# Optimization experiments

Measured on AMD Instinct MI355X. Metric: run time of the kernel, lower is better.

Reference implementation:

```python
import jax, jax.numpy as jnp
import numpy as np

N_INIT = jnp.array([17.047, 14.099, 3.625], dtype=jnp.float32)
CA_INIT = jnp.array([16.967, 12.784, 4.338], dtype=jnp.float32)
C_INIT = jnp.array([15.685, 12.755, 5.133], dtype=jnp.float32)


def _unit(x):
    return x / (jnp.linalg.norm(x, axis=-1, keepdims=True) + 1e-8)


def _place_dihedral(a, b, c, bond_angle, bond_length, torsion):
    # a,b,c: [B,3]; bond_angle/bond_length/torsion: [B]
    ab = b - a
    bc = _unit(c - b)
    cr = jnp.cross(ab, bc)
    crn = jnp.linalg.norm(cr, axis=-1, keepdims=True)
    n_main = _unit(cr)
    # collinear fallback (per-element; almost never triggers for real angles)
    perp = jnp.zeros_like(bc).at[..., 0].set(1.0)
    ct = jnp.cross(bc, perp)
    ctn = jnp.linalg.norm(ct, axis=-1, keepdims=True)
    perp2 = jnp.where(ctn < 1e-6, jnp.zeros_like(bc).at[..., 1].set(1.0), perp)
    n_fb = _unit(jnp.cross(bc, perp2))
    n = jnp.where(crn < 1e-6, n_fb, n_main)
    nbc = jnp.cross(n, bc)
    m = jnp.stack([bc, nbc, n], axis=-1)  # [B,3,3]
    d_local = jnp.stack([
        -bond_length * jnp.cos(bond_angle),
        bond_length * jnp.cos(torsion) * jnp.sin(bond_angle),
        bond_length * jnp.sin(torsion) * jnp.sin(bond_angle),
    ], axis=-1)  # [B,3]
    d = jnp.einsum('bij,bj->bi', m, d_local)
    return d + c


def _nerf_build(phi, psi, omega, bond_lengths, bond_angles):
    B, L = phi.shape
    init = jnp.broadcast_to(jnp.stack([N_INIT, CA_INIT, C_INIT]), (B, 3, 3))
    # per-step params, leading axis = residue index i in [0, L-2]
    xs = (
        psi[:, :L - 1].T,                 # psi_i
        omega[:, :L - 1].T,               # omega_i
        phi[:, 1:].T,                     # phi_{i+1}
        bond_lengths[:, :L - 1, 2].T,     # C-N length
        bond_lengths[:, :L - 1, 0].T,     # N-CA length
        bond_lengths[:, :L - 1, 1].T,     # CA-C length
        bond_angles[:, :L - 1, 1].T,      # CA-C-N angle
        bond_angles[:, :L - 1, 2].T,      # C-N-CA angle
        bond_angles[:, :L - 1, 0].T,      # N-CA-C angle
    )

    def step(prev, x):
        psi_i, omega_i, phi_i, len_cn, len_nca, len_cac, ang_cacn, ang_cnca, ang_ncac = x
        a, b, c = prev[:, 0], prev[:, 1], prev[:, 2]
        n = _place_dihedral(a, b, c, ang_cacn, len_cn, psi_i)
        ca = _place_dihedral(b, c, n, ang_cnca, len_nca, omega_i)
        cc = _place_dihedral(c, n, ca, ang_ncac, len_cac, phi_i)
        new = jnp.stack([n, ca, cc], axis=1)  # [B,3,3]
        return new, new

    _, outs = jax.lax.scan(step, init, xs)  # [L-1,B,3,3]
    rest = outs.transpose(1, 0, 2, 3).reshape(B, 3 * (L - 1), 3)
    return jnp.concatenate([init, rest], axis=1)  # [B, 3L, 3]


def setup_inputs() -> dict:
    key = jax.random.key(0)
    k0, k1, k2, k3, k4 = jax.random.split(key, 5)
    B, L = 4096, 512
    phi = jax.random.normal(k0, (B, L), dtype=jnp.float32)
    psi = jax.random.normal(k1, (B, L), dtype=jnp.float32)
    omega = jax.random.normal(k2, (B, L), dtype=jnp.float32)
    # realistic positive bond lengths (~1.0-1.5 A) and bond angles (~1.5-2.3 rad)
    bond_lengths = 1.0 + 0.5 * jax.random.uniform(k3, (B, L, 3), dtype=jnp.float32)
    bond_angles = 1.5 + 0.8 * jax.random.uniform(k4, (B, L, 3), dtype=jnp.float32)
    return {"phi": phi, "psi": psi, "omega": omega,
            "bond_lengths": bond_lengths, "bond_angles": bond_angles}


def reference(phi, psi, omega, bond_lengths, bond_angles):
    return _nerf_build(phi, psi, omega, bond_lengths, bond_angles)
```

## Files before the change

### kernel.cpp

```cpp
#include <hip/hip_runtime.h>
#include <math.h>


#define LCH 512

struct Xf { float r[9]; float t[3]; };

__device__ __forceinline__ Xf xf_compose(const Xf& A, const Xf& B) {
  Xf C;
#pragma unroll
  for (int i = 0; i < 3; ++i) {
    float a0 = A.r[3*i+0], a1 = A.r[3*i+1], a2 = A.r[3*i+2];
    C.r[3*i+0] = a0*B.r[0] + a1*B.r[3] + a2*B.r[6];
    C.r[3*i+1] = a0*B.r[1] + a1*B.r[4] + a2*B.r[7];
    C.r[3*i+2] = a0*B.r[2] + a1*B.r[5] + a2*B.r[8];
    C.t[i]     = a0*B.t[0] + a1*B.t[1] + a2*B.t[2] + A.t[i];
  }
  return C;
}

__device__ __forceinline__ void xf_step(Xf& P, float theta, float len, float tau) {
  float st, ct, sx, cx;
  __sincosf(theta, &st, &ct);
  __sincosf(tau, &sx, &cx);
  float ux = -ct, uy = cx*st, uz = sx*st;
  float v0 = -st, v1 = -ct*cx, v2 = -ct*sx;
  float c00 = P.r[0]*ux + P.r[1]*uy + P.r[2]*uz;
  float c10 = P.r[3]*ux + P.r[4]*uy + P.r[5]*uz;
  float c20 = P.r[6]*ux + P.r[7]*uy + P.r[8]*uz;
  float c01 = P.r[0]*v0 + P.r[1]*v1 + P.r[2]*v2;
  float c11 = P.r[3]*v0 + P.r[4]*v1 + P.r[5]*v2;
  float c21 = P.r[6]*v0 + P.r[7]*v1 + P.r[8]*v2;
  float c02 = P.r[2]*cx - P.r[1]*sx;
  float c12 = P.r[5]*cx - P.r[4]*sx;
  float c22 = P.r[8]*cx - P.r[7]*sx;
  P.t[0] += len*c00; P.t[1] += len*c10; P.t[2] += len*c20;
  P.r[0]=c00; P.r[1]=c01; P.r[2]=c02;
  P.r[3]=c10; P.r[4]=c11; P.r[5]=c12;
  P.r[6]=c20; P.r[7]=c21; P.r[8]=c22;
}

__device__ __forceinline__ void xf_set_delta(Xf& P, float theta, float len, float tau) {
  float st, ct, sx, cx;
  __sincosf(theta, &st, &ct);
  __sincosf(tau, &sx, &cx);
  float ux = -ct, uy = cx*st, uz = sx*st;
  P.r[0]=ux; P.r[1]=-st;    P.r[2]=0.f;
  P.r[3]=uy; P.r[4]=-ct*cx; P.r[5]=-sx;
  P.r[6]=uz; P.r[7]=-ct*sx; P.r[8]=cx;
  P.t[0]=len*ux; P.t[1]=len*uy; P.t[2]=len*uz;
}

__device__ __forceinline__ void xf_identity(Xf& A) {
  A.r[0]=1.f; A.r[1]=0.f; A.r[2]=0.f;
  A.r[3]=0.f; A.r[4]=1.f; A.r[5]=0.f;
  A.r[6]=0.f; A.r[7]=0.f; A.r[8]=1.f;
  A.t[0]=0.f; A.t[1]=0.f; A.t[2]=0.f;
}

__device__ __forceinline__ Xf xf_shfl_up(const Xf& P, int d) {
  Xf O;
#pragma unroll
  for (int i = 0; i < 9; ++i) O.r[i] = __shfl_up(P.r[i], d, 64);
#pragma unroll
  for (int i = 0; i < 3; ++i) O.t[i] = __shfl_up(P.t[i], d, 64);
  return O;
}

#define REP(f) (A.r[3*((f)%3)+0]*sx[(f)/3] + A.r[3*((f)%3)+1]*sy[(f)/3] \
              + A.r[3*((f)%3)+2]*sz[(f)/3] + A.t[(f)%3])

__global__ __launch_bounds__(128) void nerf_r14_kernel(
    const float* __restrict__ g_phi, const float* __restrict__ g_psi,
    const float* __restrict__ g_omg, const float* __restrict__ g_bl,
    const float* __restrict__ g_ba, float* __restrict__ g_out)
{
  __shared__ float s_tot[12];
  __shared__ float s_out[4608];

  const int t    = threadIdx.x;
  const int lane = t & 63;
  const int wave = t >> 6;
  const int chain = blockIdx.x;

  const float* phir = g_phi + (size_t)chain * LCH;
  const float* psir = g_psi + (size_t)chain * LCH;
  const float* omgr = g_omg + (size_t)chain * LCH;
  const float* blr  = g_bl  + (size_t)chain * (LCH*3);
  const float* bar  = g_ba  + (size_t)chain * (LCH*3);

  const int j4  = 4 * t;
  const int b12 = 12 * t;

  float4 vps = *(const float4*)(psir + j4);
  float4 vom = *(const float4*)(omgr + j4);
  float4 vph = *(const float4*)(phir + j4);
  float4 l0  = *(const float4*)(blr + b12);
  float4 l1  = *(const float4*)(blr + b12 + 4);
  float4 l2  = *(const float4*)(blr + b12 + 8);
  float4 a0  = *(const float4*)(bar + b12);
  float4 a1  = *(const float4*)(bar + b12 + 4);
  float4 a2  = *(const float4*)(bar + b12 + 8);

  float psN  = __shfl_up(vps.w, 1, 64);
  float omN  = __shfl_up(vom.w, 1, 64);
  float blN0 = __shfl_up(l2.y, 1, 64);
  float blN1 = __shfl_up(l2.z, 1, 64);
  float blN2 = __shfl_up(l2.w, 1, 64);
  float baN0 = __shfl_up(a2.y, 1, 64);
  float baN1 = __shfl_up(a2.z, 1, 64);
  float baN2 = __shfl_up(a2.w, 1, 64);
  if (lane == 0 && t != 0) {
    psN  = psir[j4 - 1];
    omN  = omgr[j4 - 1];
    blN0 = blr[b12 - 3]; blN1 = blr[b12 - 2]; blN2 = blr[b12 - 1];
    baN0 = bar[b12 - 3]; baN1 = bar[b12 - 2]; baN2 = bar[b12 - 1];
  }

  float PS[4] = { psN, vps.x, vps.y, vps.z };
  float OM[4] = { omN, vom.x, vom.y, vom.z };
  float PH[4] = { vph.x, vph.y, vph.z, vph.w };
  float BL[12] = { blN0, blN1, blN2, l0.x, l0.y, l0.z, l0.w,
                   l1.x, l1.y, l1.z, l1.w, l2.x };
  float BA[12] = { baN0, baN1, baN2, a0.x, a0.y, a0.z, a0.w,
                   a1.x, a1.y, a1.z, a1.w, a2.x };

  Xf P;
  float sx[12], sy[12], sz[12];
#pragma unroll
  for (int k = 0; k < 12; ++k) {
    const int m = k / 3, a = k - 3*m;
    float th, ln, ta;
    if (a == 0)      { th = BA[3*m+1]; ln = BL[3*m+2]; ta = PS[m]; }
    else if (a == 1) { th = BA[3*m+2]; ln = BL[3*m+0]; ta = OM[m]; }
    else             { th = BA[3*m+0]; ln = BL[3*m+1]; ta = PH[m]; }
    if (k == 0) xf_set_delta(P, th, ln, ta);
    else        xf_step(P, th, ln, ta);
    sx[k] = P.t[0]; sy[k] = P.t[1]; sz[k] = P.t[2];
    if (k == 2 && t == 0) xf_identity(P);
  }

#pragma unroll
  for (int d = 1; d < 64; d <<= 1) {
    Xf O = xf_shfl_up(P, d);
    if (lane >= d) P = xf_compose(O, P);
  }

  if (wave == 0 && lane == 63) {
#pragma unroll
    for (int i = 0; i < 9; ++i) s_tot[i] = P.r[i];
#pragma unroll
    for (int i = 0; i < 3; ++i) s_tot[9+i] = P.t[i];
  }
  Xf E = xf_shfl_up(P, 1);
  __syncthreads();

  Xf A;
  {
    const float ax=17.047f, ay=14.099f, az=3.625f;
    const float bx_=16.967f, by_=12.784f, bz_=4.338f;
    const float cx_=15.685f, cy_=12.755f, cz_=5.133f;
    float abx=bx_-ax, aby=by_-ay, abz=bz_-az;
    float vx=cx_-bx_, vy=cy_-by_, vz=cz_-bz_;
    float vn = sqrtf(vx*vx+vy*vy+vz*vz) + 1e-8f;
    vx/=vn; vy/=vn; vz/=vn;
    float crx = aby*vz - abz*vy;
    float cry = abz*vx - abx*vz;
    float crz = abx*vy - aby*vx;
    float cn = sqrtf(crx*crx+cry*cry+crz*crz) + 1e-8f;
    float nx=crx/cn, ny=cry/cn, nz=crz/cn;
    float mx = ny*vz - nz*vy;
    float my = nz*vx - nx*vz;
    float mz = nx*vy - ny*vx;
    A.r[0]=vx; A.r[1]=mx; A.r[2]=nx;
    A.r[3]=vy; A.r[4]=my; A.r[5]=ny;
    A.r[6]=vz; A.r[7]=mz; A.r[8]=nz;
    A.t[0]=cx_; A.t[1]=cy_; A.t[2]=cz_;
  }
  if (wave == 1) {
    Xf T;
#pragma unroll
    for (int i = 0; i < 9; ++i) T.r[i] = s_tot[i];
#pragma unroll
    for (int i = 0; i < 3; ++i) T.t[i] = s_tot[9+i];
    A = xf_compose(A, T);
  }
  if (lane > 0) A = xf_compose(A, E);

#pragma unroll
  for (int q = 0; q < 9; ++q) {
    float4 v;
    v.x = REP(4*q + 0);
    v.y = REP(4*q + 1);
    v.z = REP(4*q + 2);
    v.w = REP(4*q + 3);
    if (t == 0) {
      if (q == 0) { v.x=17.047f; v.y=14.099f; v.z=3.625f;  v.w=16.967f; }
      if (q == 1) { v.x=12.784f; v.y=4.338f;  v.z=15.685f; v.w=12.755f; }
      if (q == 2) { v.x=5.133f; }
    }
    *(float4*)(s_out + 36*t + 4*q) = v;
  }
  __syncthreads();

  float* orow = g_out + (size_t)chain * 4608;
#pragma unroll
  for (int p = 0; p < 9; ++p) {
    const int g = 512*p + 4*t;
    float4 v = *(const float4*)(s_out + g);
    *(float4*)(orow + g) = v;
  }
}

extern "C" void kernel_launch(void* const* d_in, const int* in_sizes, int n_in,
                              void* d_out, int out_size, void* d_ws, size_t ws_size,
                              hipStream_t stream) {
  const float* phi = (const float*)d_in[0];
  const float* psi = (const float*)d_in[1];
  const float* omg = (const float*)d_in[2];
  const float* bl  = (const float*)d_in[3];
  const float* ba  = (const float*)d_in[4];
  float* out = (float*)d_out;
  const int B = in_sizes[0] / LCH;
  hipLaunchKernelGGL(nerf_r14_kernel, dim3(B), dim3(128), 0, stream,
                     phi, psi, omg, bl, ba, out);
}
```

Before: 142.4 us.

## Split per-thread 12-step serial chain into four independent 3-step chains

Each thread's 12 sequential transform steps are replaced by four independent 3-step chains, one per residue. These are composed as a small balanced tree, and per-chain anchor transforms are precomputed for placing the atoms. This cuts the serial dependency depth so the independent chains can interleave instruction-level parallelism. The cost is extra compose operations and higher register pressure from holding four transforms live.

```diff
diff --git a/kernel.cpp b/kernel.cpp
--- a/kernel.cpp
+++ b/kernel.cpp
@@ -67,10 +67,22 @@
   return O;
 }
 
-#define REP(f) (A.r[3*((f)%3)+0]*sx[(f)/3] + A.r[3*((f)%3)+1]*sy[(f)/3] \
-              + A.r[3*((f)%3)+2]*sz[(f)/3] + A.t[(f)%3])
-
-__global__ __launch_bounds__(128) void nerf_r14_kernel(
+#define CSTEP(P, m, k, ax, ay, az) do { \
+    float th_, ln_, ta_; \
+    if      ((k) == 0) { th_ = BA[3*(m)+1]; ln_ = BL[3*(m)+2]; ta_ = PS[m]; } \
+    else if ((k) == 1) { th_ = BA[3*(m)+2]; ln_ = BL[3*(m)+0]; ta_ = OM[m]; } \
+    else               { th_ = BA[3*(m)+0]; ln_ = BL[3*(m)+1]; ta_ = PH[m]; } \
+    if ((k) == 0) xf_set_delta(P, th_, ln_, ta_); \
+    else          xf_step(P, th_, ln_, ta_); \
+    ax[k] = P.t[0]; ay[k] = P.t[1]; az[k] = P.t[2]; \
+  } while (0)
+
+#define REPF(f) (AP[(f)/9].r[3*((f)%3)+0]*px[(f)/9][((f)%9)/3] \
+               + AP[(f)/9].r[3*((f)%3)+1]*py[(f)/9][((f)%9)/3] \
+               + AP[(f)/9].r[3*((f)%3)+2]*pz[(f)/9][((f)%9)/3] \
+               + AP[(f)/9].t[(f)%3])
+
+__global__ __launch_bounds__(128) void nerf_r16_kernel(
     const float* __restrict__ g_phi, const float* __restrict__ g_psi,
     const float* __restrict__ g_omg, const float* __restrict__ g_bl,
     const float* __restrict__ g_ba, float* __restrict__ g_out)
@@ -125,20 +137,20 @@
   float BA[12] = { baN0, baN1, baN2, a0.x, a0.y, a0.z, a0.w,
                    a1.x, a1.y, a1.z, a1.w, a2.x };
 
-  Xf P;
-  float sx[12], sy[12], sz[12];
-#pragma unroll
-  for (int k = 0; k < 12; ++k) {
-    const int m = k / 3, a = k - 3*m;
-    float th, ln, ta;
-    if (a == 0)      { th = BA[3*m+1]; ln = BL[3*m+2]; ta = PS[m]; }
-    else if (a == 1) { th = BA[3*m+2]; ln = BL[3*m+0]; ta = OM[m]; }
-    else             { th = BA[3*m+0]; ln = BL[3*m+1]; ta = PH[m]; }
-    if (k == 0) xf_set_delta(P, th, ln, ta);
-    else        xf_step(P, th, ln, ta);
-    sx[k] = P.t[0]; sy[k] = P.t[1]; sz[k] = P.t[2];
-    if (k == 2 && t == 0) xf_identity(P);
-  }
+  Xf P0, P1, P2, P3;
+  float px[4][3], py[4][3], pz[4][3];
+#pragma unroll
+  for (int k = 0; k < 3; ++k) {
+    CSTEP(P0, 0, k, px[0], py[0], pz[0]);
+    CSTEP(P1, 1, k, px[1], py[1], pz[1]);
+    CSTEP(P2, 2, k, px[2], py[2], pz[2]);
+    CSTEP(P3, 3, k, px[3], py[3], pz[3]);
+  }
+  if (t == 0) xf_identity(P0);
+
+  Xf P01 = xf_compose(P0, P1);
+  Xf P23 = xf_compose(P2, P3);
+  Xf P   = xf_compose(P01, P23);
 
 #pragma unroll
   for (int d = 1; d < 64; d <<= 1) {
@@ -187,13 +199,19 @@
   }
   if (lane > 0) A = xf_compose(A, E);
 
+  Xf AP[4];
+  AP[0] = A;
+  AP[1] = xf_compose(A, P0);
+  AP[2] = xf_compose(A, P01);
+  AP[3] = xf_compose(AP[2], P2);
+
 #pragma unroll
   for (int q = 0; q < 9; ++q) {
     float4 v;
-    v.x = REP(4*q + 0);
-    v.y = REP(4*q + 1);
-    v.z = REP(4*q + 2);
-    v.w = REP(4*q + 3);
+    v.x = REPF(4*q + 0);
+    v.y = REPF(4*q + 1);
+    v.z = REPF(4*q + 2);
+    v.w = REPF(4*q + 3);
     if (t == 0) {
       if (q == 0) { v.x=17.047f; v.y=14.099f; v.z=3.625f;  v.w=16.967f; }
       if (q == 1) { v.x=12.784f; v.y=4.338f;  v.z=15.685f; v.w=12.755f; }
@@ -222,6 +240,6 @@
   const float* ba  = (const float*)d_in[4];
   float* out = (float*)d_out;
   const int B = in_sizes[0] / LCH;
-  hipLaunchKernelGGL(nerf_r14_kernel, dim3(B), dim3(128), 0, stream,
+  hipLaunchKernelGGL(nerf_r16_kernel, dim3(B), dim3(128), 0, stream,
                      phi, psi, omg, bl, ba, out);
 }
```

Result: no change. 143.9 us (+1.0%).
